# Performance work log

Hardware: AMD Instinct MI355X
Metric: run time of the kernel (lower is better)

## Reference

```python
import jax, jax.numpy as jnp
import numpy as np

B, IN, OUT, ZD = 128, 1024, 1024, 128
A_MIN = 0.2


def setup_inputs() -> dict:
    key = jax.random.key(0)
    ks = jax.random.split(key, 8)
    x = jax.random.normal(ks[0], (B, IN), dtype=jnp.float32)
    z = jax.random.normal(ks[1], (B, ZD), dtype=jnp.float32)
    base_weight = jax.random.normal(ks[2], (OUT, IN), dtype=jnp.float32) * (2.0 / IN) ** 0.5
    # nn.Linear(z_dim, out*in): weight [out*in, z_dim], bias [out*in]
    lim_w = 1.0 / np.sqrt(ZD)
    dw_W = jax.random.uniform(ks[3], (OUT * IN, ZD), minval=-lim_w, maxval=lim_w, dtype=jnp.float32)
    dw_b = jax.random.uniform(ks[4], (OUT * IN,), minval=-lim_w, maxval=lim_w, dtype=jnp.float32)
    base_bias = jnp.zeros((OUT,), dtype=jnp.float32)
    db_W = jax.random.uniform(ks[5], (OUT, ZD), minval=-lim_w, maxval=lim_w, dtype=jnp.float32)
    db_b = jax.random.uniform(ks[6], (OUT,), minval=-lim_w, maxval=lim_w, dtype=jnp.float32)
    s = jnp.asarray(2.0, dtype=jnp.float32)
    return {"x": x, "z": z, "base_weight": base_weight, "dw_W": dw_W, "dw_b": dw_b,
            "base_bias": base_bias, "db_W": db_W, "db_b": db_b, "s": s}


def reference(x, z, base_weight, dw_W, dw_b, base_bias, db_W, db_b, s):
    # eval mode: a = a_min * sigmoid(s)
    a = A_MIN * jax.nn.sigmoid(s)
    # hypernetwork head: delta_w = Linear(z) -> [B, OUT, IN]
    delta_w = (jnp.einsum('bz,oz->bo', z, dw_W) + dw_b).reshape(x.shape[0], OUT, IN)
    # per-sample blended weight
    w = a * base_weight[None, :, :] + (1.0 - a) * delta_w  # [B, OUT, IN]
    # batched matvec
    out = jnp.einsum('boi,bi->bo', w, x)
    # blended bias
    delta_b = jnp.einsum('bz,oz->bo', z, db_W) + db_b  # [B, OUT]
    b = a * base_bias + (1.0 - a) * delta_b
    return out + b
```

## Files before the change

### kernel.cpp

```cpp
#include <hip/hip_runtime.h>
#include <cmath>

#define Bsz   128
#define INsz  1024
#define OUTsz 1024
#define ZDsz  128

typedef __bf16 bf16x8 __attribute__((ext_vector_type(8)));
typedef float  floatx4 __attribute__((ext_vector_type(4)));

__global__ __launch_bounds__(512) void small_terms_kernel(
    const float* __restrict__ x, const float* __restrict__ z,
    const float* __restrict__ W, const float* __restrict__ dwb,
    const float* __restrict__ bb, const float* __restrict__ dbW,
    const float* __restrict__ dbb, const float* __restrict__ s,
    float* __restrict__ out)
{
    int t = threadIdx.x;
    int b = t & 127;
    int osub = __builtin_amdgcn_readfirstlane(t >> 7);
    int o = blockIdx.x * 4 + osub;

    float a = 0.2f / (1.f + __expf(-s[0]));
    float one_a = 1.f - a;

    const float4* W4 = reinterpret_cast<const float4*>(W   + (size_t)o * INsz);
    const float4* d4 = reinterpret_cast<const float4*>(dwb + (size_t)o * INsz);
    const float4* x4 = reinterpret_cast<const float4*>(x   + (size_t)b * INsz);

    float acc = a * bb[o] + one_a * dbb[o];
    #pragma unroll 4
    for (int i = 0; i < INsz / 4; ++i) {
        float4 wv = W4[i], dv = d4[i], xv = x4[i];
        acc += (a * wv.x + one_a * dv.x) * xv.x;
        acc += (a * wv.y + one_a * dv.y) * xv.y;
        acc += (a * wv.z + one_a * dv.z) * xv.z;
        acc += (a * wv.w + one_a * dv.w) * xv.w;
    }

    const float4* db4 = reinterpret_cast<const float4*>(dbW + (size_t)o * ZDsz);
    const float4* z4  = reinterpret_cast<const float4*>(z   + (size_t)b * ZDsz);
    float accz = 0.f;
    #pragma unroll 4
    for (int i = 0; i < ZDsz / 4; ++i) {
        float4 wv = db4[i], zv = z4[i];
        accz += wv.x * zv.x + wv.y * zv.y + wv.z * zv.z + wv.w * zv.w;
    }
    acc += one_a * accz;

    out[(size_t)b * OUTsz + o] = acc;
}

__global__ __launch_bounds__(256, 1) void hyper_main_kernel(
    const float* __restrict__ x, const float* __restrict__ z,
    const float* __restrict__ dwW, const float* __restrict__ s,
    float* __restrict__ out)
{
    __shared__ __align__(16) __bf16 zt[128 * 136];
    __shared__ __align__(16) float  xt[128 * 20];
    __shared__ float oacc[16 * 128];

    int t    = threadIdx.x;
    int lane = t & 63;
    int wave = t >> 6;
    int quad = lane >> 4;
    int l15  = lane & 15;

    float one_a = 1.f - 0.2f / (1.f + __expf(-s[0]));

    {
        int b = t >> 1;
        int half = (t & 1) * 64;
        const float4* zrow = reinterpret_cast<const float4*>(z + (size_t)b * ZDsz + half);
        __bf16* dst = &zt[b * 136 + half];
        #pragma unroll
        for (int j = 0; j < 16; ++j) {
            float4 v = zrow[j];
            dst[j*4+0] = (__bf16)v.x; dst[j*4+1] = (__bf16)v.y;
            dst[j*4+2] = (__bf16)v.z; dst[j*4+3] = (__bf16)v.w;
        }
    }
    #pragma unroll
    for (int j = 0; j < 8; ++j) oacc[t * 8 + j] = 0.f;
    __syncthreads();

    bf16x8 bfrag[8][4];
    #pragma unroll
    for (int sj = 0; sj < 8; ++sj)
        #pragma unroll
        for (int k = 0; k < 4; ++k)
            bfrag[sj][k] = *reinterpret_cast<const bf16x8*>(
                &zt[(sj * 16 + l15) * 136 + k * 32 + quad * 8]);

    int otile = blockIdx.x * 16;
    int ibase = blockIdx.y * 256;

    for (int it = 0; it < 16; ++it) {
        int i0 = ibase + it * 16;
        {
            int b = t >> 1;
            int part = (t & 1) * 8;
            const float* xr = x + (size_t)b * INsz + i0 + part;
            float* dst = &xt[b * 20 + part];
            #pragma unroll
            for (int j = 0; j < 8; ++j) dst[j] = one_a * xr[j];
        }
        __syncthreads();

        #pragma unroll 1
        for (int c = 0; c < 4; ++c) {
            int o = otile + wave * 4 + c;
            const float* abase = dwW + ((size_t)o * INsz + i0 + l15) * ZDsz + quad * 8;

            float av[4][8];
            #pragma unroll
            for (int k = 0; k < 4; ++k) {
                float4 lo = *reinterpret_cast<const float4*>(abase + k * 32);
                float4 hi = *reinterpret_cast<const float4*>(abase + k * 32 + 4);
                av[k][0]=lo.x; av[k][1]=lo.y; av[k][2]=lo.z; av[k][3]=lo.w;
                av[k][4]=hi.x; av[k][5]=hi.y; av[k][6]=hi.z; av[k][7]=hi.w;
            }
            bf16x8 afrag[4];
            #pragma unroll
            for (int k = 0; k < 4; ++k)
                #pragma unroll
                for (int j = 0; j < 8; ++j) afrag[k][j] = (__bf16)av[k][j];

            #pragma unroll
            for (int sj = 0; sj < 8; ++sj) {
                floatx4 cf = {0.f, 0.f, 0.f, 0.f};
                #pragma unroll
                for (int k = 0; k < 4; ++k)
                    cf = __builtin_amdgcn_mfma_f32_16x16x32_bf16(afrag[k], bfrag[sj][k], cf, 0, 0, 0);
                const floatx4 xv = *reinterpret_cast<const floatx4*>(&xt[(sj * 16 + l15) * 20 + quad * 4]);
                float p = cf[0]*xv[0] + cf[1]*xv[1] + cf[2]*xv[2] + cf[3]*xv[3];
                p += __shfl_xor(p, 16);
                p += __shfl_xor(p, 32);
                if (lane < 16) oacc[(wave * 4 + c) * 128 + sj * 16 + l15] += p;
            }
        }
        __syncthreads();
    }

    {
        int b = t >> 1;
        int og = (t & 1) * 8;
        #pragma unroll
        for (int j = 0; j < 8; ++j)
            atomicAdd(&out[(size_t)b * OUTsz + otile + og + j], oacc[(og + j) * 128 + b]);
    }
}

extern "C" void kernel_launch(void* const* d_in, const int* in_sizes, int n_in,
                              void* d_out, int out_size, void* d_ws, size_t ws_size,
                              hipStream_t stream) {
    (void)in_sizes; (void)n_in; (void)d_ws; (void)ws_size; (void)out_size;
    const float* x   = (const float*)d_in[0];
    const float* z   = (const float*)d_in[1];
    const float* W   = (const float*)d_in[2];
    const float* dwW = (const float*)d_in[3];
    const float* dwb = (const float*)d_in[4];
    const float* bb  = (const float*)d_in[5];
    const float* dbW = (const float*)d_in[6];
    const float* dbb = (const float*)d_in[7];
    const float* s   = (const float*)d_in[8];
    float* out = (float*)d_out;

    small_terms_kernel<<<dim3(OUTsz / 4), 512, 0, stream>>>(x, z, W, dwb, bb, dbW, dbb, s, out);
    hyper_main_kernel<<<dim3(OUTsz / 16, 4), 256, 0, stream>>>(x, z, dwW, s, out);
}
```

Measured before the change: 794.0 us.

## Fuse small-terms kernel into hypernetwork MFMA kernel and double i-split grid

Removes the separate small_terms kernel and folds its base-weight, delta-bias and bias-head contributions into the main MFMA kernel. Each MFMA result is offset by the per-element dwb + (a/(1-a))*W term, and the whole sum is scaled by (1-a) at the end. The bias head is computed with MFMA by the blockIdx.y==0 blocks. The x tile is no longer staged in shared memory and is read directly from global memory, which removes per-iteration barriers. The grid doubles along IN (8 splits of 128) with 2 blocks/CU launch bounds, and a memset zeroes the output before the atomics. The risks are more atomic traffic, uncoalesced global x loads, and a ratio that is only well-defined while a<1.

```diff
diff --git a/kernel.cpp b/kernel.cpp
--- a/kernel.cpp
+++ b/kernel.cpp
@@ -9,55 +9,14 @@
 typedef __bf16 bf16x8 __attribute__((ext_vector_type(8)));
 typedef float  floatx4 __attribute__((ext_vector_type(4)));
 
-__global__ __launch_bounds__(512) void small_terms_kernel(
+__global__ __launch_bounds__(256, 2) void hyper_fused_kernel(
     const float* __restrict__ x, const float* __restrict__ z,
-    const float* __restrict__ W, const float* __restrict__ dwb,
-    const float* __restrict__ bb, const float* __restrict__ dbW,
-    const float* __restrict__ dbb, const float* __restrict__ s,
-    float* __restrict__ out)
-{
-    int t = threadIdx.x;
-    int b = t & 127;
-    int osub = __builtin_amdgcn_readfirstlane(t >> 7);
-    int o = blockIdx.x * 4 + osub;
-
-    float a = 0.2f / (1.f + __expf(-s[0]));
-    float one_a = 1.f - a;
-
-    const float4* W4 = reinterpret_cast<const float4*>(W   + (size_t)o * INsz);
-    const float4* d4 = reinterpret_cast<const float4*>(dwb + (size_t)o * INsz);
-    const float4* x4 = reinterpret_cast<const float4*>(x   + (size_t)b * INsz);
-
-    float acc = a * bb[o] + one_a * dbb[o];
-    #pragma unroll 4
-    for (int i = 0; i < INsz / 4; ++i) {
-        float4 wv = W4[i], dv = d4[i], xv = x4[i];
-        acc += (a * wv.x + one_a * dv.x) * xv.x;
-        acc += (a * wv.y + one_a * dv.y) * xv.y;
-        acc += (a * wv.z + one_a * dv.z) * xv.z;
-        acc += (a * wv.w + one_a * dv.w) * xv.w;
-    }
-
-    const float4* db4 = reinterpret_cast<const float4*>(dbW + (size_t)o * ZDsz);
-    const float4* z4  = reinterpret_cast<const float4*>(z   + (size_t)b * ZDsz);
-    float accz = 0.f;
-    #pragma unroll 4
-    for (int i = 0; i < ZDsz / 4; ++i) {
-        float4 wv = db4[i], zv = z4[i];
-        accz += wv.x * zv.x + wv.y * zv.y + wv.z * zv.z + wv.w * zv.w;
-    }
-    acc += one_a * accz;
-
-    out[(size_t)b * OUTsz + o] = acc;
-}
-
-__global__ __launch_bounds__(256, 1) void hyper_main_kernel(
-    const float* __restrict__ x, const float* __restrict__ z,
-    const float* __restrict__ dwW, const float* __restrict__ s,
-    float* __restrict__ out)
+    const float* __restrict__ W, const float* __restrict__ dwW,
+    const float* __restrict__ dwb, const float* __restrict__ bb,
+    const float* __restrict__ dbW, const float* __restrict__ dbb,
+    const float* __restrict__ s, float* __restrict__ out)
 {
     __shared__ __align__(16) __bf16 zt[128 * 136];
-    __shared__ __align__(16) float  xt[128 * 20];
     __shared__ float oacc[16 * 128];
 
     int t    = threadIdx.x;
@@ -66,7 +25,9 @@
     int quad = lane >> 4;
     int l15  = lane & 15;
 
-    float one_a = 1.f - 0.2f / (1.f + __expf(-s[0]));
+    float a     = 0.2f / (1.f + __expf(-s[0]));
+    float one_a = 1.f - a;
+    float ratio = a / one_a;
 
     {
         int b = t >> 1;
@@ -93,38 +54,33 @@
                 &zt[(sj * 16 + l15) * 136 + k * 32 + quad * 8]);
 
     int otile = blockIdx.x * 16;
-    int ibase = blockIdx.y * 256;
+    int ibase = blockIdx.y * 128;
 
-    for (int it = 0; it < 16; ++it) {
+    for (int it = 0; it < 8; ++it) {
         int i0 = ibase + it * 16;
-        {
-            int b = t >> 1;
-            int part = (t & 1) * 8;
-            const float* xr = x + (size_t)b * INsz + i0 + part;
-            float* dst = &xt[b * 20 + part];
-            #pragma unroll
-            for (int j = 0; j < 8; ++j) dst[j] = one_a * xr[j];
-        }
-        __syncthreads();
-
         #pragma unroll 1
         for (int c = 0; c < 4; ++c) {
             int o = otile + wave * 4 + c;
+
+            float4 Wv = *reinterpret_cast<const float4*>(W   + (size_t)o * INsz + i0 + quad * 4);
+            float4 Dv = *reinterpret_cast<const float4*>(dwb + (size_t)o * INsz + i0 + quad * 4);
+
             const float* abase = dwW + ((size_t)o * INsz + i0 + l15) * ZDsz + quad * 8;
-
-            float av[4][8];
+            bf16x8 afrag[4];
             #pragma unroll
             for (int k = 0; k < 4; ++k) {
                 float4 lo = *reinterpret_cast<const float4*>(abase + k * 32);
                 float4 hi = *reinterpret_cast<const float4*>(abase + k * 32 + 4);
-                av[k][0]=lo.x; av[k][1]=lo.y; av[k][2]=lo.z; av[k][3]=lo.w;
-                av[k][4]=hi.x; av[k][5]=hi.y; av[k][6]=hi.z; av[k][7]=hi.w;
+                afrag[k][0]=(__bf16)lo.x; afrag[k][1]=(__bf16)lo.y;
+                afrag[k][2]=(__bf16)lo.z; afrag[k][3]=(__bf16)lo.w;
+                afrag[k][4]=(__bf16)hi.x; afrag[k][5]=(__bf16)hi.y;
+                afrag[k][6]=(__bf16)hi.z; afrag[k][7]=(__bf16)hi.w;
             }
-            bf16x8 afrag[4];
-            #pragma unroll
-            for (int k = 0; k < 4; ++k)
-                #pragma unroll
-                for (int j = 0; j < 8; ++j) afrag[k][j] = (__bf16)av[k][j];
+
+            float wex0 = Dv.x + ratio * Wv.x;
+            float wex1 = Dv.y + ratio * Wv.y;
+            float wex2 = Dv.z + ratio * Wv.z;
+            float wex3 = Dv.w + ratio * Wv.w;
 
             #pragma unroll
             for (int sj = 0; sj < 8; ++sj) {
@@ -132,29 +88,63 @@
                 #pragma unroll
                 for (int k = 0; k < 4; ++k)
                     cf = __builtin_amdgcn_mfma_f32_16x16x32_bf16(afrag[k], bfrag[sj][k], cf, 0, 0, 0);
-                const floatx4 xv = *reinterpret_cast<const floatx4*>(&xt[(sj * 16 + l15) * 20 + quad * 4]);
-                float p = cf[0]*xv[0] + cf[1]*xv[1] + cf[2]*xv[2] + cf[3]*xv[3];
+                const floatx4 xv = *reinterpret_cast<const floatx4*>(
+                    x + (size_t)(sj * 16 + l15) * INsz + i0 + quad * 4);
+                float p = (cf[0] + wex0) * xv[0] + (cf[1] + wex1) * xv[1]
+                        + (cf[2] + wex2) * xv[2] + (cf[3] + wex3) * xv[3];
                 p += __shfl_xor(p, 16);
                 p += __shfl_xor(p, 32);
                 if (lane < 16) oacc[(wave * 4 + c) * 128 + sj * 16 + l15] += p;
             }
         }
+    }
+
+    if (blockIdx.y == 0) {
         __syncthreads();
+        const float* abase = dbW + (size_t)(otile + l15) * ZDsz + quad * 8;
+        bf16x8 afrag[4];
+        #pragma unroll
+        for (int k = 0; k < 4; ++k) {
+            float4 lo = *reinterpret_cast<const float4*>(abase + k * 32);
+            float4 hi = *reinterpret_cast<const float4*>(abase + k * 32 + 4);
+            afrag[k][0]=(__bf16)lo.x; afrag[k][1]=(__bf16)lo.y;
+            afrag[k][2]=(__bf16)lo.z; afrag[k][3]=(__bf16)lo.w;
+            afrag[k][4]=(__bf16)hi.x; afrag[k][5]=(__bf16)hi.y;
+            afrag[k][6]=(__bf16)hi.z; afrag[k][7]=(__bf16)hi.w;
+        }
+        float4 bbv  = *reinterpret_cast<const float4*>(bb  + otile + quad * 4);
+        float4 dbbv = *reinterpret_cast<const float4*>(dbb + otile + quad * 4);
+        float bias0 = ratio * bbv.x + dbbv.x, bias1 = ratio * bbv.y + dbbv.y;
+        float bias2 = ratio * bbv.z + dbbv.z, bias3 = ratio * bbv.w + dbbv.w;
+        #pragma unroll
+        for (int u = 0; u < 2; ++u) {
+            int sj = wave * 2 + u;
+            floatx4 cf = {0.f, 0.f, 0.f, 0.f};
+            #pragma unroll
+            for (int k = 0; k < 4; ++k)
+                cf = __builtin_amdgcn_mfma_f32_16x16x32_bf16(afrag[k], bfrag[sj][k], cf, 0, 0, 0);
+            oacc[(quad * 4 + 0) * 128 + sj * 16 + l15] += cf[0] + bias0;
+            oacc[(quad * 4 + 1) * 128 + sj * 16 + l15] += cf[1] + bias1;
+            oacc[(quad * 4 + 2) * 128 + sj * 16 + l15] += cf[2] + bias2;
+            oacc[(quad * 4 + 3) * 128 + sj * 16 + l15] += cf[3] + bias3;
+        }
     }
+    __syncthreads();
 
     {
         int b = t >> 1;
         int og = (t & 1) * 8;
         #pragma unroll
         for (int j = 0; j < 8; ++j)
-            atomicAdd(&out[(size_t)b * OUTsz + otile + og + j], oacc[(og + j) * 128 + b]);
+            atomicAdd(&out[(size_t)b * OUTsz + otile + og + j],
+                      one_a * oacc[(og + j) * 128 + b]);
     }
 }
 
 extern "C" void kernel_launch(void* const* d_in, const int* in_sizes, int n_in,
                               void* d_out, int out_size, void* d_ws, size_t ws_size,
                               hipStream_t stream) {
-    (void)in_sizes; (void)n_in; (void)d_ws; (void)ws_size; (void)out_size;
+    (void)in_sizes; (void)n_in; (void)d_ws; (void)ws_size;
     const float* x   = (const float*)d_in[0];
     const float* z   = (const float*)d_in[1];
     const float* W   = (const float*)d_in[2];
@@ -166,6 +156,7 @@
     const float* s   = (const float*)d_in[8];
     float* out = (float*)d_out;
 
-    small_terms_kernel<<<dim3(OUTsz / 4), 512, 0, stream>>>(x, z, W, dwb, bb, dbW, dbb, s, out);
-    hyper_main_kernel<<<dim3(OUTsz / 16, 4), 256, 0, stream>>>(x, z, dwW, s, out);
+    hipMemsetAsync(out, 0, (size_t)out_size * sizeof(float), stream);
+    hyper_fused_kernel<<<dim3(OUTsz / 16, 8), 256, 0, stream>>>(
+        x, z, W, dwW, dwb, bb, dbW, dbb, s, out);
 }
```

New measurement: 737.4 us. 1.08x faster.
